# Optimization experiments

Hardware: AMD Instinct MI355X
Metric: run time of the kernel (lower is better)

The kernel has to match this reference:

```python
import jax, jax.numpy as jnp
import numpy as np

NUM_CLASS = 8192
FEAT_DIM = 512
BATCH = 131072


def setup_inputs() -> dict:
    key = jax.random.key(0)
    k1, k2, k3 = jax.random.split(key, 3)
    batch_samples = jax.random.normal(k1, (BATCH, FEAT_DIM), dtype=jnp.float32)
    class_sums = jnp.zeros((NUM_CLASS, FEAT_DIM), dtype=jnp.float32)
    targets = jax.random.randint(k2, (BATCH,), 0, NUM_CLASS, dtype=jnp.int64)
    idx = jax.random.randint(k3, (BATCH,), 0, BATCH, dtype=jnp.int64)
    return {"batch_samples": batch_samples, "class_sums": class_sums,
            "targets": targets, "idx": idx}


def reference(batch_samples, class_sums, targets, idx):
    # Original forward: for each unique label, class_sums[label] += sum of rows
    # of batch_samples with that label. This is exactly a segment-sum
    # (scatter-add by class label) accumulated into class_sums.
    # idx is unused in the forward math (kept for signature fidelity).
    inc = jax.ops.segment_sum(batch_samples, targets, num_segments=NUM_CLASS)
    return class_sums + inc  # updated class_sums buffer [num_class, feat_dim]
```

## Files before the change

kernel.cpp:

```cpp
#include <hip/hip_runtime.h>
#include <hip/hip_bf16.h>


#define FEAT 512
#define FEAT4 128
#define SCAN_THREADS 256

__global__ void k_zero(int* __restrict__ counts, int n) {
    int i = blockIdx.x * blockDim.x + threadIdx.x;
    if (i < n) counts[i] = 0;
}

__global__ void k_hist(const int* __restrict__ targets, int* __restrict__ counts, int batch) {
    int i = blockIdx.x * blockDim.x + threadIdx.x;
    if (i < batch) atomicAdd(&counts[targets[i]], 1);
}

__global__ void k_scan(const int* __restrict__ counts, int* __restrict__ offsets,
                       int* __restrict__ fill, int num_class) {
    __shared__ int sums[SCAN_THREADS];
    const int t = threadIdx.x;
    const int bins = num_class / SCAN_THREADS;
    int local[32];
    int base = t * bins;
    int s = 0;
    #pragma unroll
    for (int i = 0; i < 32; ++i) { local[i] = counts[base + i]; s += local[i]; }
    sums[t] = s;
    __syncthreads();
    for (int off = 1; off < SCAN_THREADS; off <<= 1) {
        int v = (t >= off) ? sums[t - off] : 0;
        __syncthreads();
        sums[t] += v;
        __syncthreads();
    }
    int run = sums[t] - s;
    #pragma unroll
    for (int i = 0; i < 32; ++i) {
        offsets[base + i] = run;
        fill[base + i]    = run;
        run += local[i];
    }
}

__global__ void k_scatter(const int* __restrict__ targets, int* __restrict__ fill,
                          int* __restrict__ rows, int batch) {
    int i = blockIdx.x * blockDim.x + threadIdx.x;
    if (i < batch) {
        int pos = atomicAdd(&fill[targets[i]], 1);
        rows[pos] = i;
    }
}

__global__ __launch_bounds__(128) void k_sum(const float4* __restrict__ batch,
                                             const float4* __restrict__ csums,
                                             const int* __restrict__ offsets,
                                             const int* __restrict__ counts,
                                             const int* __restrict__ rows,
                                             float4* __restrict__ out) {
    const int c = blockIdx.x;
    const int t = threadIdx.x;
    const int start = offsets[c];
    const int n     = counts[c];

    float4 acc = csums[(size_t)c * FEAT4 + t];

    __shared__ int sidx[512];
    for (int chunk = 0; chunk < n; chunk += 512) {
        const int m = min(n - chunk, 512);
        for (int j = t; j < m; j += 128) sidx[j] = rows[start + chunk + j];
        __syncthreads();
        for (int j = 0; j < m; ++j) {
            float4 v = batch[(size_t)sidx[j] * FEAT4 + t];
            acc.x += v.x; acc.y += v.y; acc.z += v.z; acc.w += v.w;
        }
        __syncthreads();
    }
    out[(size_t)c * FEAT4 + t] = acc;
}

__global__ void k_copy(const float4* __restrict__ src, float4* __restrict__ dst, int n4) {
    int i = blockIdx.x * blockDim.x + threadIdx.x;
    if (i < n4) dst[i] = src[i];
}

__global__ __launch_bounds__(128) void k_atomic(const float4* __restrict__ batch,
                                                const int* __restrict__ targets,
                                                float* __restrict__ out, int batch_n) {
    const int r = blockIdx.x;
    const int t = threadIdx.x;
    if (r >= batch_n) return;
    float4 v = batch[(size_t)r * FEAT4 + t];
    float* o = out + (size_t)targets[r] * FEAT + t * 4;
    atomicAdd(o + 0, v.x);
    atomicAdd(o + 1, v.y);
    atomicAdd(o + 2, v.z);
    atomicAdd(o + 3, v.w);
}

extern "C" void kernel_launch(void* const* d_in, const int* in_sizes, int n_in,
                              void* d_out, int out_size, void* d_ws, size_t ws_size,
                              hipStream_t stream) {
    const float* batch_samples = (const float*)d_in[0];
    const float* class_sums    = (const float*)d_in[1];
    const int*   targets       = (const int*)d_in[2];

    const int batch     = in_sizes[2];
    const int num_class = out_size / FEAT;
    float* out = (float*)d_out;

    const size_t need = (size_t)num_class * 4 * 3 + (size_t)batch * 4;
    if (ws_size >= need) {
        int* counts  = (int*)d_ws;
        int* offsets = counts + num_class;
        int* fill    = offsets + num_class;
        int* rows    = fill + num_class;

        k_zero<<<(num_class + 255) / 256, 256, 0, stream>>>(counts, num_class);
        k_hist<<<(batch + 255) / 256, 256, 0, stream>>>(targets, counts, batch);
        k_scan<<<1, SCAN_THREADS, 0, stream>>>(counts, offsets, fill, num_class);
        k_scatter<<<(batch + 255) / 256, 256, 0, stream>>>(targets, fill, rows, batch);
        k_sum<<<num_class, 128, 0, stream>>>((const float4*)batch_samples,
                                             (const float4*)class_sums,
                                             offsets, counts, rows,
                                             (float4*)out);
    } else {
        const int n4 = out_size / 4;
        k_copy<<<(n4 + 255) / 256, 256, 0, stream>>>((const float4*)class_sums,
                                                     (float4*)out, n4);
        k_atomic<<<batch, 128, 0, stream>>>((const float4*)batch_samples,
                                            targets, out, batch);
    }
}
```

Baseline: 401.9 us.

## Unroll gather loop by eight, stage scan in LDS, drop offsets array

The per-class summation loop now issues eight independent row loads before accumulating them, so more memory requests are in flight per thread. The scan kernel stages counts in padded shared memory with coalesced global loads and stores, instead of strided per-thread accesses. The separate offsets array is removed: the start index is recovered as fill minus count after the scatter. The zeroing kernel is replaced by hipMemsetAsync. The reordered additions slightly change float rounding, and the fast path now requires num_class to be a multiple of 256 and at most 8192.

```diff
diff --git a/kernel.cpp b/kernel.cpp
--- a/kernel.cpp
+++ b/kernel.cpp
@@ -6,26 +6,25 @@
 #define FEAT4 128
 #define SCAN_THREADS 256
 
-__global__ void k_zero(int* __restrict__ counts, int n) {
-    int i = blockIdx.x * blockDim.x + threadIdx.x;
-    if (i < n) counts[i] = 0;
-}
-
 __global__ void k_hist(const int* __restrict__ targets, int* __restrict__ counts, int batch) {
     int i = blockIdx.x * blockDim.x + threadIdx.x;
     if (i < batch) atomicAdd(&counts[targets[i]], 1);
 }
 
-__global__ void k_scan(const int* __restrict__ counts, int* __restrict__ offsets,
-                       int* __restrict__ fill, int num_class) {
+__global__ __launch_bounds__(SCAN_THREADS) void k_scan(const int* __restrict__ counts,
+                                                       int* __restrict__ fill,
+                                                       int num_class) {
+    __shared__ int sh[8192 + 256];
     __shared__ int sums[SCAN_THREADS];
     const int t = threadIdx.x;
     const int bins = num_class / SCAN_THREADS;
-    int local[32];
-    int base = t * bins;
+
+    for (int i = t; i < num_class; i += SCAN_THREADS) sh[i + (i >> 5)] = counts[i];
+    __syncthreads();
+
+    const int base = t * bins;
     int s = 0;
-    #pragma unroll
-    for (int i = 0; i < 32; ++i) { local[i] = counts[base + i]; s += local[i]; }
+    for (int i = 0; i < bins; ++i) { int idx = base + i; s += sh[idx + (idx >> 5)]; }
     sums[t] = s;
     __syncthreads();
     for (int off = 1; off < SCAN_THREADS; off <<= 1) {
@@ -35,12 +34,14 @@
         __syncthreads();
     }
     int run = sums[t] - s;
-    #pragma unroll
-    for (int i = 0; i < 32; ++i) {
-        offsets[base + i] = run;
-        fill[base + i]    = run;
-        run += local[i];
+    for (int i = 0; i < bins; ++i) {
+        int idx = base + i;
+        int c = sh[idx + (idx >> 5)];
+        sh[idx + (idx >> 5)] = run;
+        run += c;
     }
+    __syncthreads();
+    for (int i = t; i < num_class; i += SCAN_THREADS) fill[i] = sh[i + (i >> 5)];
 }
 
 __global__ void k_scatter(const int* __restrict__ targets, int* __restrict__ fill,
@@ -54,14 +55,14 @@
 
 __global__ __launch_bounds__(128) void k_sum(const float4* __restrict__ batch,
                                              const float4* __restrict__ csums,
-                                             const int* __restrict__ offsets,
+                                             const int* __restrict__ fill,
                                              const int* __restrict__ counts,
                                              const int* __restrict__ rows,
                                              float4* __restrict__ out) {
     const int c = blockIdx.x;
     const int t = threadIdx.x;
-    const int start = offsets[c];
-    const int n     = counts[c];
+    const int n = counts[c];
+    const int start = fill[c] - n;
 
     float4 acc = csums[(size_t)c * FEAT4 + t];
 
@@ -70,7 +71,23 @@
         const int m = min(n - chunk, 512);
         for (int j = t; j < m; j += 128) sidx[j] = rows[start + chunk + j];
         __syncthreads();
-        for (int j = 0; j < m; ++j) {
+
+        int j = 0;
+        for (; j + 8 <= m; j += 8) {
+            float4 v0 = batch[(size_t)sidx[j + 0] * FEAT4 + t];
+            float4 v1 = batch[(size_t)sidx[j + 1] * FEAT4 + t];
+            float4 v2 = batch[(size_t)sidx[j + 2] * FEAT4 + t];
+            float4 v3 = batch[(size_t)sidx[j + 3] * FEAT4 + t];
+            float4 v4 = batch[(size_t)sidx[j + 4] * FEAT4 + t];
+            float4 v5 = batch[(size_t)sidx[j + 5] * FEAT4 + t];
+            float4 v6 = batch[(size_t)sidx[j + 6] * FEAT4 + t];
+            float4 v7 = batch[(size_t)sidx[j + 7] * FEAT4 + t];
+            acc.x += ((v0.x + v1.x) + (v2.x + v3.x)) + ((v4.x + v5.x) + (v6.x + v7.x));
+            acc.y += ((v0.y + v1.y) + (v2.y + v3.y)) + ((v4.y + v5.y) + (v6.y + v7.y));
+            acc.z += ((v0.z + v1.z) + (v2.z + v3.z)) + ((v4.z + v5.z) + (v6.z + v7.z));
+            acc.w += ((v0.w + v1.w) + (v2.w + v3.w)) + ((v4.w + v5.w) + (v6.w + v7.w));
+        }
+        for (; j < m; ++j) {
             float4 v = batch[(size_t)sidx[j] * FEAT4 + t];
             acc.x += v.x; acc.y += v.y; acc.z += v.z; acc.w += v.w;
         }
@@ -109,20 +126,19 @@
     const int num_class = out_size / FEAT;
     float* out = (float*)d_out;
 
-    const size_t need = (size_t)num_class * 4 * 3 + (size_t)batch * 4;
-    if (ws_size >= need) {
-        int* counts  = (int*)d_ws;
-        int* offsets = counts + num_class;
-        int* fill    = offsets + num_class;
-        int* rows    = fill + num_class;
+    const size_t need = (size_t)num_class * 4 * 2 + (size_t)batch * 4;
+    if (ws_size >= need && (num_class % SCAN_THREADS) == 0 && num_class <= 8192) {
+        int* counts = (int*)d_ws;
+        int* fill   = counts + num_class;
+        int* rows   = fill + num_class;
 
-        k_zero<<<(num_class + 255) / 256, 256, 0, stream>>>(counts, num_class);
+        hipMemsetAsync(counts, 0, (size_t)num_class * 4, stream);
         k_hist<<<(batch + 255) / 256, 256, 0, stream>>>(targets, counts, batch);
-        k_scan<<<1, SCAN_THREADS, 0, stream>>>(counts, offsets, fill, num_class);
+        k_scan<<<1, SCAN_THREADS, 0, stream>>>(counts, fill, num_class);
         k_scatter<<<(batch + 255) / 256, 256, 0, stream>>>(targets, fill, rows, batch);
         k_sum<<<num_class, 128, 0, stream>>>((const float4*)batch_samples,
                                              (const float4*)class_sums,
-                                             offsets, counts, rows,
+                                             fill, counts, rows,
                                              (float4*)out);
     } else {
         const int n4 = out_size / 4;
```

Result: no change. 402.8 us (+0.2%).
